# Kernel tuning notes

Measured on AMD Instinct MI355X. Metric: run time of the kernel, lower is better.

## Reference

```python
import jax, jax.numpy as jnp
import numpy as np
from jax import lax

H_IMG, W_IMG = 512, 640
PX, PY = 600.0, 600.0
U0, V0 = 320.0, 256.0
BORDER = 5
CH = H_IMG - 2 * BORDER  # cropped height
CW = W_IMG - 2 * BORDER  # cropped width
N = CH * CW
# 7-tap derivative filter (as in ImageGradients)
F = jnp.array([-112.0, -913.0, -2047.0, 0.0, 2047.0, 913.0, 112.0], dtype=jnp.float32) / 8418.0


def setup_inputs() -> dict:
    key = jax.random.key(0)
    k1, k2, k3, k4 = jax.random.split(key, 4)
    B = 64
    Is = jax.random.normal(k1, (B, H_IMG, W_IMG), dtype=jnp.float32)
    Ids = jax.random.normal(k2, (B, H_IMG, W_IMG), dtype=jnp.float32)
    Zinv = jax.random.uniform(k3, (B, H_IMG, W_IMG), dtype=jnp.float32) + 0.1  # positive inverse depth
    mu = jax.random.uniform(k4, (B,), dtype=jnp.float32)
    return {"Is": Is, "Ids": Ids, "Zinv": Zinv, "mu": mu}


def _image_gradients(x):
    # x: (B, H, W). Cross-correlation with 7-tap filter (matches torch conv2d).
    b = BORDER
    xi = x[:, None, b:-b, b - 3:-(b - 3)]       # (B,1,CH,CW+6)
    yi = x[:, None, b - 3:-(b - 3), b:-b]       # (B,1,CH+6,CW)
    kx = F.reshape(1, 1, 1, 7)
    ky = F.reshape(1, 1, 7, 1)
    Ix = lax.conv_general_dilated(xi, kx, (1, 1), 'VALID')[:, 0]  # (B,CH,CW)
    Iy = lax.conv_general_dilated(yi, ky, (1, 1), 'VALID')[:, 0]  # (B,CH,CW)
    return Ix, Iy


def _dvs_forward(Is, Ids, Zinv, mu):
    b = BORDER
    B = Is.shape[0]
    # crop + flatten
    Zv = Zinv[:, b:-b, b:-b].reshape(B, N)
    Isv = Is[:, b:-b, b:-b].reshape(B, N)
    Idsv = Ids[:, b:-b, b:-b].reshape(B, N)
    Idx, Idy = _image_gradients(Ids)
    Ixv = Idx.reshape(B, N) * PX
    Iyv = Idy.reshape(B, N) * PY
    # normalized image coordinates per pixel (flattened row-major)
    xs = (jnp.arange(b, W_IMG - b, dtype=jnp.float32) - U0) / PX  # (CW,)
    ys = (jnp.arange(b, H_IMG - b, dtype=jnp.float32) - V0) / PY  # (CH,)
    xsf = jnp.tile(xs, CH)                 # (N,)
    ysf = jnp.repeat(ys, CW)               # (N,)
    xsys = xsf * ysf
    # interaction matrix columns -> (B, N, 6)
    Lsd = jnp.stack([
        Ixv * Zv,
        Iyv * Zv,
        -(xsf * Ixv + ysf * Iyv) * Zv,
        -Ixv * xsys - (1.0 + ysf ** 2) * Iyv,
        (1.0 + xsf ** 2) * Ixv + Iyv * xsys,
        Iyv * xsf - Ixv * ysf,
    ], axis=-1)
    # Gauss-Newton Hessian (B,6,6) via tall-skinny reduction
    Hsd = jnp.einsum('bni,bnj->bij', Lsd, Lsd)
    diags = jnp.diagonal(Hsd, axis1=-2, axis2=-1)        # (B,6)
    diagHsd = jnp.eye(6, dtype=Hsd.dtype) * diags[:, None, :]
    Hinv = jnp.linalg.inv(mu[:, None, None] * diagHsd + Hsd)
    e = Isv - Idsv                                        # (B,N)
    g = jnp.einsum('bni,bn->bi', Lsd, e)                  # Lsd^T e
    vc = -jnp.einsum('bij,bj->bi', Hinv, g)               # (B,6)
    return vc


def reference(Is, Ids, Zinv, mu):
    return _dvs_forward(Is, Ids, Zinv, mu)
```

## Files before the change

### kernel.cpp

```cpp
#include <hip/hip_runtime.h>
#include <math.h>


namespace {
constexpr int HI = 512, WI = 640, BRD = 5;
constexpr int RPT = 8;
constexpr int TILES = 64;
constexpr int WVS = 4;
constexpr int BPS = TILES / WVS;
constexpr int SEGS = 3;
constexpr int BLK_PER_B = SEGS * BPS;
constexpr float PXc = 600.0f, PYc = 600.0f, U0c = 320.0f, V0c = 256.0f;
constexpr float G1 = 2047.0f / 8418.0f * 600.0f;
constexpr float G2 = 913.0f  / 8418.0f * 600.0f;
constexpr float G3 = 112.0f  / 8418.0f * 600.0f;
}

__device__ __forceinline__ float elem(const float4 v, int q) {
    return q == 0 ? v.x : (q == 1 ? v.y : (q == 2 ? v.z : v.w));
}

__global__ __launch_bounds__(256) void dvs_partial(
    const float* __restrict__ Is, const float* __restrict__ Ids,
    const float* __restrict__ Zinv, float* __restrict__ ws)
{
    const int tid  = threadIdx.x;
    const int lane = tid & 63;
    const int wv   = tid >> 6;
    const int b   = blockIdx.x / BLK_PER_B;
    const int rem = blockIdx.x - b * BLK_PER_B;
    const int seg = rem / BPS;
    const int bg  = rem - seg * BPS;
    const int tile = bg * WVS + wv;
    const int r0 = BRD + tile * RPT;

    const int base = (seg == 0) ? 0   : ((seg == 1) ? 200 : 384);
    const int lo   = (seg == 0) ? 5   : ((seg == 1) ? 252 : 452);
    const int hi   = (seg == 0) ? 252 : ((seg == 1) ? 452 : 635);
    const int c0 = base + (lane << 2);

    const size_t ofs = (size_t)b * (HI * WI);
    const float* __restrict__ Ib = Is   + ofs;
    const float* __restrict__ Db = Ids  + ofs;
    const float* __restrict__ Zb = Zinv + ofs;

    float msk[4], xk[4];
#pragma unroll
    for (int q = 0; q < 4; ++q) {
        const int c = c0 + q;
        msk[q] = (c >= lo && c < hi) ? 1.0f : 0.0f;
        xk[q]  = ((float)c - U0c) * (1.0f / PXc);
    }

    float4 win[14];
#pragma unroll
    for (int j = 0; j < 14; ++j) {
        const int rr = min(r0 - 3 + j, HI - 1);
        win[j] = *(const float4*)(Db + rr * WI + c0);
    }
    float4 isb[2], zvb[2];
    {
        const int rr = min(r0, HI - 1);
        isb[0] = *(const float4*)(Ib + rr * WI + c0);
        zvb[0] = *(const float4*)(Zb + rr * WI + c0);
    }
    isb[1] = isb[0]; zvb[1] = zvb[0];

    float acc[27];
#pragma unroll
    for (int t = 0; t < 27; ++t) acc[t] = 0.0f;

    const int lm = (lane + 63) & 63, lp = (lane + 1) & 63;

#pragma unroll
    for (int k = 0; k < RPT; ++k) {
        if (k < RPT - 1) {
            const int rr = min(r0 + k + 1, HI - 1);
            isb[(k + 1) & 1] = *(const float4*)(Ib + rr * WI + c0);
            zvb[(k + 1) & 1] = *(const float4*)(Zb + rr * WI + c0);
        }
        const int rc = r0 + k;
        const float rmk = (rc < HI - BRD) ? 1.0f : 0.0f;
        const float4 a0 = win[k], a1 = win[k + 1], a2 = win[k + 2],
                     ct = win[k + 3], a4 = win[k + 4], a5 = win[k + 5],
                     a6 = win[k + 6];
        const float hl1 = __shfl(ct.w, lm);
        const float hl2 = __shfl(ct.z, lm);
        const float hl3 = __shfl(ct.y, lm);
        const float hr1 = __shfl(ct.x, lp);
        const float hr2 = __shfl(ct.y, lp);
        const float hr3 = __shfl(ct.z, lp);
        const float h[10] = {hl3, hl2, hl1, ct.x, ct.y, ct.z, ct.w,
                             hr1, hr2, hr3};
        const float yv  = ((float)rc - V0c) * (1.0f / PYc);
        const float4 isV = isb[k & 1], zV = zvb[k & 1];
#pragma unroll
        for (int q = 0; q < 4; ++q) {
            const float m  = msk[q] * rmk;
            const float Ix = fmaf(G3, h[q + 6] - h[q],
                              fmaf(G2, h[q + 5] - h[q + 1],
                                   G1 * (h[q + 4] - h[q + 2]))) * m;
            const float Iy = fmaf(G3, elem(a6, q) - elem(a0, q),
                              fmaf(G2, elem(a5, q) - elem(a1, q),
                                   G1 * (elem(a4, q) - elem(a2, q)))) * m;
            const float Z  = elem(zV, q);
            const float e  = elem(isV, q) - elem(ct, q);
            const float x  = xk[q], xy = x * yv;
            const float tt = x * Ix, uu = yv * Iy;
            float L[6];
            L[0] = Ix * Z;
            L[1] = Iy * Z;
            L[2] = -(tt + uu) * Z;
            L[3] = -(fmaf(yv, uu, Iy) + Ix * xy);
            L[4] = fmaf(x, tt, Ix) + Iy * xy;
            L[5] = Iy * x - Ix * yv;
            int t = 0;
#pragma unroll
            for (int i = 0; i < 6; ++i)
#pragma unroll
                for (int j = i; j < 6; ++j)
                    acc[t++] += L[i] * L[j];
#pragma unroll
            for (int i = 0; i < 6; ++i) acc[21 + i] += L[i] * e;
        }
    }

#pragma unroll
    for (int t = 0; t < 27; ++t) {
        float v = acc[t];
        v += __shfl_xor(v, 1);  v += __shfl_xor(v, 2);  v += __shfl_xor(v, 4);
        v += __shfl_xor(v, 8);  v += __shfl_xor(v, 16); v += __shfl_xor(v, 32);
        acc[t] = v;
    }
    float outv = acc[0];
#pragma unroll
    for (int t = 1; t < 27; ++t) if (lane == t) outv = acc[t];

    __shared__ float red[WVS][28];
    if (lane < 27) red[wv][lane] = outv;
    __syncthreads();
    if (tid < 27) {
        float s = red[0][tid] + red[1][tid] + red[2][tid] + red[3][tid];
        ws[(size_t)blockIdx.x * 27 + tid] = s;
    }
}

__global__ __launch_bounds__(128) void dvs_solve(
    const float* __restrict__ ws, const float* __restrict__ mu,
    float* __restrict__ out)
{
    const int b = blockIdx.x;
    __shared__ float sd[27][BLK_PER_B + 1];
    for (int i = threadIdx.x; i < BLK_PER_B * 27; i += 128) {
        const int s = i / 27, k = i - s * 27;
        sd[k][s] = ws[((size_t)b * BLK_PER_B + s) * 27 + k];
    }
    __syncthreads();
    __shared__ double hsum[27];
    if (threadIdx.x < 27) {
        double t = 0.0;
        for (int s = 0; s < BLK_PER_B; ++s) t += (double)sd[threadIdx.x][s];
        hsum[threadIdx.x] = t;
    }
    __syncthreads();
    if (threadIdx.x == 0) {
        double A[6][7];
        int k = 0;
        for (int i = 0; i < 6; ++i)
            for (int j = i; j < 6; ++j) { A[i][j] = hsum[k]; A[j][i] = hsum[k]; ++k; }
        const double dm = 1.0 + (double)mu[b];
        for (int i = 0; i < 6; ++i) { A[i][i] *= dm; A[i][6] = hsum[21 + i]; }
        for (int col = 0; col < 6; ++col) {
            int p = col; double best = fabs(A[col][col]);
            for (int r = col + 1; r < 6; ++r) {
                const double vv = fabs(A[r][col]);
                if (vv > best) { best = vv; p = r; }
            }
            if (p != col)
                for (int cc = col; cc < 7; ++cc) {
                    const double t = A[col][cc]; A[col][cc] = A[p][cc]; A[p][cc] = t;
                }
            const double inv = 1.0 / A[col][col];
            for (int r = col + 1; r < 6; ++r) {
                const double f = A[r][col] * inv;
                for (int cc = col + 1; cc < 7; ++cc) A[r][cc] -= f * A[col][cc];
            }
        }
        double xs[6];
        for (int i = 5; i >= 0; --i) {
            double s = A[i][6];
            for (int j = i + 1; j < 6; ++j) s -= A[i][j] * xs[j];
            xs[i] = s / A[i][i];
        }
        for (int i = 0; i < 6; ++i) out[b * 6 + i] = (float)(-xs[i]);
    }
}

extern "C" void kernel_launch(void* const* d_in, const int* in_sizes, int n_in,
                              void* d_out, int out_size, void* d_ws, size_t ws_size,
                              hipStream_t stream)
{
    const float* Is   = (const float*)d_in[0];
    const float* Ids  = (const float*)d_in[1];
    const float* Zinv = (const float*)d_in[2];
    const float* mu   = (const float*)d_in[3];
    const int B = in_sizes[3];
    float* out = (float*)d_out;
    float* ws  = (float*)d_ws;

    dvs_partial<<<B * BLK_PER_B, 256, 0, stream>>>(Is, Ids, Zinv, ws);
    dvs_solve<<<B, 128, 0, stream>>>(ws, mu, out);
}
```

Measured before the change: 58.46 us.

## Remap block IDs across XCDs, deepen Is/Z prefetch, simplify solve reduction

Block indices are permuted so that consecutive logical work groups land on the same of the eight XCDs, which should make neighbouring tiles of one image share an L2. The Is/Zinv row prefetch is deepened from two buffers to three to hide more load latency. The solve kernel drops its shared-memory staging and reads the partials directly with one 64-thread wave. The result is a mix of unrelated locality, latency and launch-size tweaks, and the deeper prefetch costs extra registers per thread.

```diff
diff --git a/kernel.cpp b/kernel.cpp
--- a/kernel.cpp
+++ b/kernel.cpp
@@ -27,8 +27,13 @@
     const int tid  = threadIdx.x;
     const int lane = tid & 63;
     const int wv   = tid >> 6;
-    const int b   = blockIdx.x / BLK_PER_B;
-    const int rem = blockIdx.x - b * BLK_PER_B;
+    int wg = blockIdx.x;
+    if ((gridDim.x & 7) == 0) {
+        const int chunk = gridDim.x >> 3;
+        wg = (blockIdx.x & 7) * chunk + (blockIdx.x >> 3);
+    }
+    const int b   = wg / BLK_PER_B;
+    const int rem = wg - b * BLK_PER_B;
     const int seg = rem / BPS;
     const int bg  = rem - seg * BPS;
     const int tile = bg * WVS + wv;
@@ -58,13 +63,16 @@
         const int rr = min(r0 - 3 + j, HI - 1);
         win[j] = *(const float4*)(Db + rr * WI + c0);
     }
-    float4 isb[2], zvb[2];
+    float4 isb[3], zvb[3];
     {
-        const int rr = min(r0, HI - 1);
-        isb[0] = *(const float4*)(Ib + rr * WI + c0);
-        zvb[0] = *(const float4*)(Zb + rr * WI + c0);
-    }
-    isb[1] = isb[0]; zvb[1] = zvb[0];
+        const int ra = min(r0, HI - 1);
+        const int rb = min(r0 + 1, HI - 1);
+        isb[0] = *(const float4*)(Ib + ra * WI + c0);
+        zvb[0] = *(const float4*)(Zb + ra * WI + c0);
+        isb[1] = *(const float4*)(Ib + rb * WI + c0);
+        zvb[1] = *(const float4*)(Zb + rb * WI + c0);
+    }
+    isb[2] = isb[0]; zvb[2] = zvb[0];
 
     float acc[27];
 #pragma unroll
@@ -74,10 +82,10 @@
 
 #pragma unroll
     for (int k = 0; k < RPT; ++k) {
-        if (k < RPT - 1) {
-            const int rr = min(r0 + k + 1, HI - 1);
-            isb[(k + 1) & 1] = *(const float4*)(Ib + rr * WI + c0);
-            zvb[(k + 1) & 1] = *(const float4*)(Zb + rr * WI + c0);
+        if (k < RPT - 2) {
+            const int rr = min(r0 + k + 2, HI - 1);
+            isb[(k + 2) % 3] = *(const float4*)(Ib + rr * WI + c0);
+            zvb[(k + 2) % 3] = *(const float4*)(Zb + rr * WI + c0);
         }
         const int rc = r0 + k;
         const float rmk = (rc < HI - BRD) ? 1.0f : 0.0f;
@@ -93,7 +101,7 @@
         const float h[10] = {hl3, hl2, hl1, ct.x, ct.y, ct.z, ct.w,
                              hr1, hr2, hr3};
         const float yv  = ((float)rc - V0c) * (1.0f / PYc);
-        const float4 isV = isb[k & 1], zV = zvb[k & 1];
+        const float4 isV = isb[k % 3], zV = zvb[k % 3];
 #pragma unroll
         for (int q = 0; q < 4; ++q) {
             const float m  = msk[q] * rmk;
@@ -141,29 +149,25 @@
     __syncthreads();
     if (tid < 27) {
         float s = red[0][tid] + red[1][tid] + red[2][tid] + red[3][tid];
-        ws[(size_t)blockIdx.x * 27 + tid] = s;
-    }
-}
-
-__global__ __launch_bounds__(128) void dvs_solve(
+        ws[(size_t)wg * 27 + tid] = s;
+    }
+}
+
+__global__ __launch_bounds__(64) void dvs_solve(
     const float* __restrict__ ws, const float* __restrict__ mu,
     float* __restrict__ out)
 {
     const int b = blockIdx.x;
-    __shared__ float sd[27][BLK_PER_B + 1];
-    for (int i = threadIdx.x; i < BLK_PER_B * 27; i += 128) {
-        const int s = i / 27, k = i - s * 27;
-        sd[k][s] = ws[((size_t)b * BLK_PER_B + s) * 27 + k];
+    const int lane = threadIdx.x;
+    __shared__ double hsum[27];
+    if (lane < 27) {
+        double t = 0.0;
+        for (int s = 0; s < BLK_PER_B; ++s)
+            t += (double)ws[((size_t)b * BLK_PER_B + s) * 27 + lane];
+        hsum[lane] = t;
     }
     __syncthreads();
-    __shared__ double hsum[27];
-    if (threadIdx.x < 27) {
-        double t = 0.0;
-        for (int s = 0; s < BLK_PER_B; ++s) t += (double)sd[threadIdx.x][s];
-        hsum[threadIdx.x] = t;
-    }
-    __syncthreads();
-    if (threadIdx.x == 0) {
+    if (lane == 0) {
         double A[6][7];
         int k = 0;
         for (int i = 0; i < 6; ++i)
@@ -209,5 +213,5 @@
     float* ws  = (float*)d_ws;
 
     dvs_partial<<<B * BLK_PER_B, 256, 0, stream>>>(Is, Ids, Zinv, ws);
-    dvs_solve<<<B, 128, 0, stream>>>(ws, mu, out);
-}
+    dvs_solve<<<B, 64, 0, stream>>>(ws, mu, out);
+}
```

Result: faster. 56.96 us (-2.6%).
